# Performance work log

Hardware: AMD Instinct MI355X
Metric: run time of the kernel (lower is better)

## Reference

```python
import jax, jax.numpy as jnp
import numpy as np

D_MODEL = 1024
N_HEADS = 16
D_HEAD = 64
BATCH = 4
SEQ = 2048
NEG = -1000000000.0


def setup_inputs() -> dict:
    key = jax.random.key(0)
    k1, k2, k3, k4, k5 = jax.random.split(key, 5)
    x = jax.random.normal(k1, (BATCH, SEQ, D_MODEL), dtype=jnp.float32)
    std = 0.02
    wq = jax.random.normal(k2, (N_HEADS, D_HEAD, D_MODEL), dtype=jnp.float32) * std
    wk = jax.random.normal(k3, (N_HEADS, D_HEAD, D_MODEL), dtype=jnp.float32) * std
    wv = jax.random.normal(k4, (N_HEADS, D_HEAD, D_MODEL), dtype=jnp.float32) * std
    wo = jax.random.normal(k5, (D_MODEL, N_HEADS * D_HEAD), dtype=jnp.float32) * std
    return {"x": x, "wq": wq, "wk": wk, "wv": wv, "wo": wo}


def reference(x, wq, wk, wv, wo):
    # x: [b, s, d_model]; wq/wk/wv: [h, d_head, d_model]; wo: [d_model, h*d_head]
    b, s, _ = x.shape
    scale = jnp.sqrt(jnp.asarray(D_HEAD, x.dtype))
    q = jnp.einsum('bsd,hed->bhse', x, wq)
    k = jnp.einsum('bsd,hed->bhse', x, wk)
    v = jnp.einsum('bsd,hed->bhse', x, wv)
    scores = jnp.einsum('bhse,bhte->bhst', q, k) / scale
    causal_mask = jnp.triu(jnp.ones((s, s), dtype=bool), k=1)
    scores = jnp.where(causal_mask, jnp.asarray(NEG, scores.dtype), scores)
    weights = jax.nn.softmax(scores, axis=-1)
    heads = jnp.einsum('bhst,bhte->bhse', weights, v)  # [b, h, s, d_head]
    concat = heads.transpose(0, 2, 1, 3).reshape(b, s, N_HEADS * D_HEAD)
    return concat @ wo.T
```

## Files before the change

kernel.cpp:

```cpp
#include <hip/hip_runtime.h>


#define DEV __device__ __forceinline__

typedef __attribute__((ext_vector_type(8))) __bf16 bf16x8;
typedef __attribute__((ext_vector_type(4))) float f32x4;
typedef unsigned short u16;

struct alignas(8) U16x4 { u16 x, y, z, w; };

DEV u16 f2bf(float f) {
  unsigned int u = __builtin_bit_cast(unsigned int, f);
  u = u + 0x7FFFu + ((u >> 16) & 1u);
  return (u16)(u >> 16);
}

DEV unsigned cvt_pk_bf16(float a, float b) {
  unsigned r;
  asm("v_cvt_pk_bf16_f32 %0, %1, %2" : "=v"(r) : "v"(a), "v"(b));
  return r;
}

DEV f32x4 mfma16(uint2 a, uint2 b, f32x4 c) {
  f32x4 d;
  asm("v_mfma_f32_16x16x16_bf16 %0, %1, %2, %3" : "=v"(d) : "v"(a), "v"(b), "v"(c));
  return d;
}

DEV void gload_lds16(const void* g, void* l) {
  __builtin_amdgcn_global_load_lds(
      (const __attribute__((address_space(1))) unsigned int*)g,
      (__attribute__((address_space(3))) unsigned int*)l, 16, 0, 0);
}

DEV void waitvm(int n) {
  if (n >= 12)     asm volatile("s_waitcnt vmcnt(12)" ::: "memory");
  else if (n == 8) asm volatile("s_waitcnt vmcnt(8)" ::: "memory");
  else if (n == 4) asm volatile("s_waitcnt vmcnt(4)" ::: "memory");
  else             asm volatile("s_waitcnt vmcnt(0)" ::: "memory");
}

__global__ __launch_bounds__(256) void cast_all_kernel(
    const float* __restrict__ x, const float* __restrict__ wq,
    const float* __restrict__ wk, const float* __restrict__ wv,
    const float* __restrict__ wo, u16* __restrict__ xb,
    u16* __restrict__ wqkvb, u16* __restrict__ wob) {
  const int i = blockIdx.x * blockDim.x + threadIdx.x;
  const float* src;
  U16x4* dst;
  if (i < 2097152) {
    src = x + (size_t)i * 4;
    dst = reinterpret_cast<U16x4*>(xb) + i;
  } else if (i < 2883584) {
    const int j = i - 2097152;
    const int sel = j >> 18;
    const float* s = sel == 0 ? wq : sel == 1 ? wk : wv;
    src = s + (size_t)(j & 262143) * 4;
    dst = reinterpret_cast<U16x4*>(wqkvb) + j;
  } else {
    const int j = i - 2883584;
    src = wo + (size_t)j * 4;
    dst = reinterpret_cast<U16x4*>(wob) + j;
  }
  const float4 v = *reinterpret_cast<const float4*>(src);
  *dst = U16x4{f2bf(v.x), f2bf(v.y), f2bf(v.z), f2bf(v.w)};
}

template <int MODE, int NBN>
__global__ __launch_bounds__(256, 2) void gemm_bt(
    const u16* __restrict__ A, const u16* __restrict__ B,
    void* __restrict__ C0, u16* __restrict__ vtp, int N) {
  constexpr int K = 1024;
  const int d = blockIdx.x;
  const int chunk = gridDim.x >> 3;
  const int vg = (d & 7) * chunk + (d >> 3);
  const int bn = vg % NBN, bm = vg / NBN;
  const int tid = threadIdx.x;
  const int w = tid >> 6, lane = tid & 63, lo = lane & 15, hi = lane >> 4;
  const int wm = w >> 1, wn = w & 1;

  __shared__ char lds[65536];

  const u16* Ag = A + (size_t)(bm * 128) * K;
  const u16* Bg = B + (size_t)(bn * 128) * K;

  f32x4 acc[4][4] = {};

  auto stage = [&](int ring, int k0) {
#pragma unroll
    for (int j = 0; j < 2; ++j) {
      const int L = j * 256 + tid, r = L >> 2, c = (L & 3) ^ (r & 3);
      gload_lds16(Ag + (size_t)r * K + k0 + c * 8, lds + ring * 16384 + j * 4096 + w * 1024);
      gload_lds16(Bg + (size_t)r * K + k0 + c * 8, lds + ring * 16384 + 8192 + j * 4096 + w * 1024);
    }
  };

  stage(0, 0);
  stage(1, 32);
  stage(2, 64);

#pragma unroll
  for (int t = 0; t < 32; ++t) {
    if (t + 3 < 32) stage((t + 3) & 3, (t + 3) * 32);
    waitvm(4 * (31 - t < 3 ? 31 - t : 3));
    __builtin_amdgcn_sched_barrier(0);
    __builtin_amdgcn_s_barrier();

    const int ro = (t & 3) * 16384;
    bf16x8 af[4], bfr[4];
#pragma unroll
    for (int m = 0; m < 4; ++m) {
      const int r = wm * 64 + m * 16 + lo;
      const int p = hi ^ (lo & 3);
      af[m] = *reinterpret_cast<const bf16x8*>(lds + ro + r * 64 + p * 16);
    }
#pragma unroll
    for (int n = 0; n < 4; ++n) {
      const int r = wn * 64 + n * 16 + lo;
      const int p = hi ^ (lo & 3);
      bfr[n] = *reinterpret_cast<const bf16x8*>(lds + ro + 8192 + r * 64 + p * 16);
    }
    __builtin_amdgcn_s_setprio(1);
#pragma unroll
    for (int m = 0; m < 4; ++m)
#pragma unroll
      for (int n = 0; n < 4; ++n)
        acc[m][n] = __builtin_amdgcn_mfma_f32_16x16x32_bf16(af[m], bfr[n], acc[m][n], 0, 0, 0);
    __builtin_amdgcn_s_setprio(0);
    asm volatile("s_waitcnt lgkmcnt(0)" ::: "memory");
    __builtin_amdgcn_sched_barrier(0);
    __builtin_amdgcn_s_barrier();
  }

  const int colW = bn * 128 + wn * 64;
  const int rowW = bm * 128 + wm * 64;
  if (MODE == 0) {
    float* C = (float*)C0;
#pragma unroll
    for (int m = 0; m < 4; ++m)
#pragma unroll
      for (int n = 0; n < 4; ++n) {
        const int col = colW + n * 16 + lo;
        const int rb = rowW + m * 16 + hi * 4;
#pragma unroll
        for (int rg = 0; rg < 4; ++rg)
          C[(size_t)(rb + rg) * N + col] = acc[m][n][rg];
      }
  } else {
    u16* qkvp = (u16*)C0;
    if (bn * 128 < 2048) {
      const float qs = (bn < 8) ? 0.18033688011112042f : 1.0f;
#pragma unroll
      for (int m = 0; m < 4; ++m)
#pragma unroll
        for (int n = 0; n < 4; ++n) {
          const int col = colW + n * 16 + lo;
          const int rb = rowW + m * 16 + hi * 4;
#pragma unroll
          for (int rg = 0; rg < 4; ++rg)
            qkvp[(size_t)(rb + rg) * 2048 + col] = f2bf(acc[m][n][rg] * qs);
        }
    } else {
#pragma unroll
      for (int m = 0; m < 4; ++m)
#pragma unroll
        for (int n = 0; n < 4; ++n) {
          const int col = colW + n * 16 + lo;
          const int idx = col - 2048;
          const int hh = idx >> 6, e = idx & 63;
          const int rb = rowW + m * 16 + hi * 4;
          const int bb = rb >> 11, s = rb & 2047;
          U16x4 v4{f2bf(acc[m][n][0]), f2bf(acc[m][n][1]),
                   f2bf(acc[m][n][2]), f2bf(acc[m][n][3])};
          *reinterpret_cast<U16x4*>(vtp + ((size_t)((bb * 16 + hh) * 64 + e)) * 2048 + s) = v4;
        }
    }
  }
}

__global__ __launch_bounds__(512, 4) void attn_kernel(
    const u16* __restrict__ qkv, const u16* __restrict__ vt, u16* __restrict__ heads) {
  const int dd = blockIdx.x;
  const int vg = (dd & 7) * 64 + (dd >> 3);
  const int bx = vg & 7, bh = vg >> 3;
  const int b = bh >> 4, h = bh & 15;
  const int tid = threadIdx.x;
  const int w = tid >> 6, lane = tid & 63, lo = lane & 15, hi = lane >> 4;

  __shared__ char lds[81920];
  char* sQP = lds;
  char* sK  = lds + 16384;
  char* sV  = lds + 49152;

  const u16* Kg = qkv + (size_t)(b * 2048) * 2048 + 1024 + h * 64;
  const u16* Vg = vt + (size_t)bh * 64 * 2048;

  const int kr = tid >> 3, kc_ = (tid & 7) ^ (kr & 7);
  const int vr = tid >> 4, vc_ = (tid & 15) ^ (vr & 7);
  auto stageKV = [&](int buf, int kv0) {
#pragma unroll
    for (int it = 0; it < 2; ++it) {
      gload_lds16(Kg + (size_t)(kv0 + it * 64 + kr) * 2048 + kc_ * 8,
                  sK + buf * 16384 + it * 8192 + w * 1024);
      gload_lds16(Vg + (size_t)(it * 32 + vr) * 2048 + kv0 + vc_ * 8,
                  sV + buf * 16384 + it * 8192 + w * 1024);
    }
  };

  const int qloc = w * 16 + lo;

  for (int rep = 0; rep < 2; ++rep) {
    const int qt = rep ? (15 - bx) : bx;
    const u16* Qg = qkv + (size_t)(b * 2048 + qt * 128) * 2048 + h * 64;

#pragma unroll
    for (int it = 0; it < 2; ++it)
      gload_lds16(Qg + (size_t)(it * 64 + kr) * 2048 + kc_ * 8, sQP + it * 8192 + w * 1024);
    stageKV(0, 0);
    __syncthreads();

    bf16x8 qf[2];
#pragma unroll
    for (int kc = 0; kc < 2; ++kc) {
      const int p = (kc * 4 + hi) ^ (lo & 7);
      qf[kc] = *reinterpret_cast<const bf16x8*>(sQP + qloc * 128 + p * 16);
    }

    f32x4 lvec = {};
    f32x4 oacc[4] = {};

    const int nt = qt + 1;

    auto step = [&](int t, int cur) {
      if (t + 1 < nt) stageKV(cur ^ 1, (t + 1) * 128);
      f32x4 sa[8] = {};
      __builtin_amdgcn_s_setprio(1);
#pragma unroll
      for (int kc = 0; kc < 2; ++kc) {
#pragma unroll
        for (int n = 0; n < 8; ++n) {
          const int r = n * 16 + lo;
          const int p = (kc * 4 + hi) ^ (lo & 7);
          const bf16x8 kf = *reinterpret_cast<const bf16x8*>(sK + cur * 16384 + r * 128 + p * 16);
          sa[n] = __builtin_amdgcn_mfma_f32_16x16x32_bf16(kf, qf[kc], sa[n], 0, 0, 0);
        }
      }
      __builtin_amdgcn_s_setprio(0);

      if (t == nt - 1) {
#pragma unroll
        for (int n = 0; n < 8; ++n)
#pragma unroll
          for (int rg = 0; rg < 4; ++rg)
            if (n * 16 + hi * 4 + rg > qloc) sa[n][rg] = -1e9f;
      }

#pragma unroll
      for (int n = 0; n < 8; ++n)
#pragma unroll
        for (int rg = 0; rg < 4; ++rg) sa[n][rg] = exp2f(sa[n][rg]);
      lvec += ((sa[0] + sa[1]) + (sa[2] + sa[3])) + ((sa[4] + sa[5]) + (sa[6] + sa[7]));

      __builtin_amdgcn_s_setprio(1);
#pragma unroll
      for (int n = 0; n < 8; ++n) {
        const uint2 pb{cvt_pk_bf16(sa[n][0], sa[n][1]), cvt_pk_bf16(sa[n][2], sa[n][3])};
        const int sb = (((2 * n + (hi >> 1)) ^ (lo & 7)) << 4) + ((hi & 1) << 3);
#pragma unroll
        for (int ne = 0; ne < 4; ++ne) {
          const uint2 vf = *reinterpret_cast<const uint2*>(
              sV + cur * 16384 + (ne * 16 + lo) * 256 + sb);
          oacc[ne] = mfma16(vf, pb, oacc[ne]);
        }
      }
      __builtin_amdgcn_s_setprio(0);
      __syncthreads();
    };

    for (int i = 0; i < nt; i += 2) {
      step(i, 0);
      if (i + 1 < nt) step(i + 1, 1);
    }

    float lsum = (lvec[0] + lvec[1]) + (lvec[2] + lvec[3]);
    lsum += __shfl_xor(lsum, 16);
    lsum += __shfl_xor(lsum, 32);
    const float inv = 1.0f / lsum;
    const int q = qt * 128 + qloc;
    u16* dst = heads + (size_t)(b * 2048 + q) * 1024 + h * 64;
#pragma unroll
    for (int ne = 0; ne < 4; ++ne) {
      const unsigned r0 = cvt_pk_bf16(oacc[ne][0] * inv, oacc[ne][1] * inv);
      const unsigned r1 = cvt_pk_bf16(oacc[ne][2] * inv, oacc[ne][3] * inv);
      *reinterpret_cast<uint2*>(dst + ne * 16 + hi * 4) = uint2{r0, r1};
    }
  }
}

extern "C" void kernel_launch(void* const* d_in, const int* in_sizes, int n_in,
                              void* d_out, int out_size, void* d_ws, size_t ws_size,
                              hipStream_t stream) {
  const float* x  = (const float*)d_in[0];
  const float* wq = (const float*)d_in[1];
  const float* wk = (const float*)d_in[2];
  const float* wv = (const float*)d_in[3];
  const float* wo = (const float*)d_in[4];

  char* ws = (char*)d_ws;
  u16* xb    = (u16*)(ws);
  u16* wqkvb = (u16*)(ws + 16777216);
  u16* wob   = (u16*)(ws + 23068672);
  u16* qkv   = (u16*)(ws + 25165824);
  u16* vtp   = (u16*)(ws + 58720256);
  u16* heads = (u16*)(ws + 75497472);

  cast_all_kernel<<<12288, 256, 0, stream>>>(x, wq, wk, wv, wo, xb, wqkvb, wob);

  gemm_bt<1, 24><<<1536, 256, 0, stream>>>(xb, wqkvb, qkv, vtp, 3072);
  attn_kernel<<<512, 512, 0, stream>>>(qkv, vtp, heads);
  gemm_bt<0, 8><<<512, 256, 0, stream>>>(heads, wob, d_out, nullptr, 1024);
}
```

Before: 169.6 us.

## Rewrite attention with 32x32x16 MFMA, smaller blocks and 32-key tiles

The attention kernel is restructured to use v_mfma_f32_32x32x16_bf16 with permlane32_swap to relayout P, smaller 128-thread blocks (2048 blocks), 32-key KV tiles staged into 16KB LDS, and Q kept in registers loaded directly from global. Causal work past each wave's diagonal is skipped per wave. The goal is higher occupancy, better load balance from more, smaller blocks ordered by descending q-tile, and fewer MFMA instructions per FLOP. The cost is more barriers per unit of work, since each 32-key step now has its own sync. The GEMM waitcnt helper is also inlined.

```diff
diff --git a/kernel.cpp b/kernel.cpp
--- a/kernel.cpp
+++ b/kernel.cpp
@@ -5,6 +5,8 @@
 
 typedef __attribute__((ext_vector_type(8))) __bf16 bf16x8;
 typedef __attribute__((ext_vector_type(4))) float f32x4;
+typedef __attribute__((ext_vector_type(16))) float f32x16;
+typedef __attribute__((ext_vector_type(2))) unsigned uint32x2;
 typedef unsigned short u16;
 
 struct alignas(8) U16x4 { u16 x, y, z, w; };
@@ -21,23 +23,15 @@
   return r;
 }
 
-DEV f32x4 mfma16(uint2 a, uint2 b, f32x4 c) {
-  f32x4 d;
-  asm("v_mfma_f32_16x16x16_bf16 %0, %1, %2, %3" : "=v"(d) : "v"(a), "v"(b), "v"(c));
-  return d;
+DEV f32x16 mfma32(bf16x8 a, bf16x8 b, f32x16 c) {
+  asm("v_mfma_f32_32x32x16_bf16 %0, %1, %2, %0" : "+v"(c) : "v"(a), "v"(b));
+  return c;
 }
 
 DEV void gload_lds16(const void* g, void* l) {
   __builtin_amdgcn_global_load_lds(
       (const __attribute__((address_space(1))) unsigned int*)g,
       (__attribute__((address_space(3))) unsigned int*)l, 16, 0, 0);
-}
-
-DEV void waitvm(int n) {
-  if (n >= 12)     asm volatile("s_waitcnt vmcnt(12)" ::: "memory");
-  else if (n == 8) asm volatile("s_waitcnt vmcnt(8)" ::: "memory");
-  else if (n == 4) asm volatile("s_waitcnt vmcnt(4)" ::: "memory");
-  else             asm volatile("s_waitcnt vmcnt(0)" ::: "memory");
 }
 
 __global__ __launch_bounds__(256) void cast_all_kernel(
@@ -102,7 +96,10 @@
 #pragma unroll
   for (int t = 0; t < 32; ++t) {
     if (t + 3 < 32) stage((t + 3) & 3, (t + 3) * 32);
-    waitvm(4 * (31 - t < 3 ? 31 - t : 3));
+    if (t < 29)      asm volatile("s_waitcnt vmcnt(12)" ::: "memory");
+    else if (t == 29) asm volatile("s_waitcnt vmcnt(8)" ::: "memory");
+    else if (t == 30) asm volatile("s_waitcnt vmcnt(4)" ::: "memory");
+    else              asm volatile("s_waitcnt vmcnt(0)" ::: "memory");
     __builtin_amdgcn_sched_barrier(0);
     __builtin_amdgcn_s_barrier();
 
@@ -178,123 +175,124 @@
   }
 }
 
-__global__ __launch_bounds__(512, 4) void attn_kernel(
+__global__ __launch_bounds__(128, 4) void attn_kernel(
     const u16* __restrict__ qkv, const u16* __restrict__ vt, u16* __restrict__ heads) {
-  const int dd = blockIdx.x;
-  const int vg = (dd & 7) * 64 + (dd >> 3);
-  const int bx = vg & 7, bh = vg >> 3;
-  const int b = bh >> 4, h = bh & 15;
+  const int x = blockIdx.x & 7;
+  const int i = blockIdx.x >> 3;
+  const int bh = x + 8 * (i & 7);
+  const int qt = 31 - (i >> 3);
+  const int b = bh >> 4, hh = bh & 15;
   const int tid = threadIdx.x;
-  const int w = tid >> 6, lane = tid & 63, lo = lane & 15, hi = lane >> 4;
-
-  __shared__ char lds[81920];
-  char* sQP = lds;
-  char* sK  = lds + 16384;
-  char* sV  = lds + 49152;
-
-  const u16* Kg = qkv + (size_t)(b * 2048) * 2048 + 1024 + h * 64;
+  const int w = tid >> 6, l = tid & 63, l31 = l & 31, h = l >> 5;
+
+  __shared__ char lds[16384];
+  char* sK = lds;
+  char* sV = lds + 8192;
+
+  const u16* Kg = qkv + (size_t)(b * 2048) * 2048 + 1024 + hh * 64;
   const u16* Vg = vt + (size_t)bh * 64 * 2048;
 
-  const int kr = tid >> 3, kc_ = (tid & 7) ^ (kr & 7);
-  const int vr = tid >> 4, vc_ = (tid & 15) ^ (vr & 7);
-  auto stageKV = [&](int buf, int kv0) {
-#pragma unroll
-    for (int it = 0; it < 2; ++it) {
-      gload_lds16(Kg + (size_t)(kv0 + it * 64 + kr) * 2048 + kc_ * 8,
-                  sK + buf * 16384 + it * 8192 + w * 1024);
-      gload_lds16(Vg + (size_t)(it * 32 + vr) * 2048 + kv0 + vc_ * 8,
-                  sV + buf * 16384 + it * 8192 + w * 1024);
+  int kR[2], kC[2], vE[2], vC[2];
+#pragma unroll
+  for (int j = 0; j < 2; ++j) {
+    const int L = j * 128 + w * 64 + l;
+    kR[j] = L >> 3; kC[j] = (L & 7) ^ (kR[j] & 7);
+    vE[j] = L >> 2; vC[j] = (L & 3) ^ ((vE[j] >> 1) & 3);
+  }
+  auto stage = [&](int buf, int t) {
+    const size_t kv0 = (size_t)t * 32;
+#pragma unroll
+    for (int j = 0; j < 2; ++j) {
+      gload_lds16(Kg + (kv0 + kR[j]) * 2048 + kC[j] * 8, sK + buf * 4096 + j * 2048 + w * 1024);
+      gload_lds16(Vg + (size_t)vE[j] * 2048 + kv0 + vC[j] * 8, sV + buf * 4096 + j * 2048 + w * 1024);
     }
   };
 
-  const int qloc = w * 16 + lo;
-
-  for (int rep = 0; rep < 2; ++rep) {
-    const int qt = rep ? (15 - bx) : bx;
-    const u16* Qg = qkv + (size_t)(b * 2048 + qt * 128) * 2048 + h * 64;
-
-#pragma unroll
-    for (int it = 0; it < 2; ++it)
-      gload_lds16(Qg + (size_t)(it * 64 + kr) * 2048 + kc_ * 8, sQP + it * 8192 + w * 1024);
-    stageKV(0, 0);
-    __syncthreads();
-
-    bf16x8 qf[2];
-#pragma unroll
-    for (int kc = 0; kc < 2; ++kc) {
-      const int p = (kc * 4 + hi) ^ (lo & 7);
-      qf[kc] = *reinterpret_cast<const bf16x8*>(sQP + qloc * 128 + p * 16);
-    }
-
-    f32x4 lvec = {};
-    f32x4 oacc[4] = {};
-
-    const int nt = qt + 1;
-
-    auto step = [&](int t, int cur) {
-      if (t + 1 < nt) stageKV(cur ^ 1, (t + 1) * 128);
-      f32x4 sa[8] = {};
+  const int gq = qt * 64 + w * 32 + l31;
+  const u16* Qrow = qkv + (size_t)(b * 2048 + gq) * 2048 + hh * 64 + 8 * h;
+  bf16x8 qfr[4];
+#pragma unroll
+  for (int c = 0; c < 4; ++c)
+    qfr[c] = *reinterpret_cast<const bf16x8*>(Qrow + 16 * c);
+
+  float lsum = 0.f;
+  f32x16 oacc[2] = {};
+
+  const int nt = 2 * (qt + 1);
+  const int wqmax = qt * 64 + w * 32 + 31;
+
+  stage(0, 0);
+  __syncthreads();
+
+  auto step = [&](int t, int cur) {
+    if (t + 1 < nt) stage(cur ^ 1, t + 1);
+    if (t * 32 <= wqmax) {
+      f32x16 sa = {};
       __builtin_amdgcn_s_setprio(1);
 #pragma unroll
-      for (int kc = 0; kc < 2; ++kc) {
-#pragma unroll
-        for (int n = 0; n < 8; ++n) {
-          const int r = n * 16 + lo;
-          const int p = (kc * 4 + hi) ^ (lo & 7);
-          const bf16x8 kf = *reinterpret_cast<const bf16x8*>(sK + cur * 16384 + r * 128 + p * 16);
-          sa[n] = __builtin_amdgcn_mfma_f32_16x16x32_bf16(kf, qf[kc], sa[n], 0, 0, 0);
+      for (int c = 0; c < 4; ++c) {
+        const int slot = (2 * c + h) ^ (l31 & 7);
+        const bf16x8 kf = *reinterpret_cast<const bf16x8*>(sK + cur * 4096 + l31 * 128 + slot * 16);
+        sa = mfma32(kf, qfr[c], sa);
+      }
+      __builtin_amdgcn_s_setprio(0);
+
+      if (t >= nt - 2) {
+        const int thr = gq - t * 32;
+#pragma unroll
+        for (int r = 0; r < 16; ++r) {
+          const int rowloc = (r & 3) + 8 * (r >> 2) + 4 * h;
+          if (rowloc > thr) sa[r] = -1e9f;
         }
       }
-      __builtin_amdgcn_s_setprio(0);
-
-      if (t == nt - 1) {
-#pragma unroll
-        for (int n = 0; n < 8; ++n)
-#pragma unroll
-          for (int rg = 0; rg < 4; ++rg)
-            if (n * 16 + hi * 4 + rg > qloc) sa[n][rg] = -1e9f;
+
+#pragma unroll
+      for (int r = 0; r < 16; ++r) sa[r] = exp2f(sa[r]);
+      float rs = 0.f;
+#pragma unroll
+      for (int r = 0; r < 16; ++r) rs += sa[r];
+      lsum += rs;
+
+#pragma unroll
+      for (int sc = 0; sc < 2; ++sc) {
+        const unsigned w0 = cvt_pk_bf16(sa[8 * sc + 0], sa[8 * sc + 1]);
+        const unsigned w1 = cvt_pk_bf16(sa[8 * sc + 2], sa[8 * sc + 3]);
+        const unsigned w2 = cvt_pk_bf16(sa[8 * sc + 4], sa[8 * sc + 5]);
+        const unsigned w3 = cvt_pk_bf16(sa[8 * sc + 6], sa[8 * sc + 7]);
+        const uint32x2 s02 = __builtin_amdgcn_permlane32_swap(w0, w2, false, false);
+        const uint32x2 s13 = __builtin_amdgcn_permlane32_swap(w1, w3, false, false);
+        union { unsigned u[4]; bf16x8 v; } pb;
+        pb.u[0] = s02.x; pb.u[1] = s13.x; pb.u[2] = s02.y; pb.u[3] = s13.y;
+        __builtin_amdgcn_s_setprio(1);
+#pragma unroll
+        for (int ne = 0; ne < 2; ++ne) {
+          const int e = ne * 32 + l31;
+          const int slot = (2 * sc + h) ^ ((e >> 1) & 3);
+          const bf16x8 vf = *reinterpret_cast<const bf16x8*>(sV + cur * 4096 + e * 64 + slot * 16);
+          oacc[ne] = mfma32(vf, pb.v, oacc[ne]);
+        }
+        __builtin_amdgcn_s_setprio(0);
       }
-
-#pragma unroll
-      for (int n = 0; n < 8; ++n)
-#pragma unroll
-        for (int rg = 0; rg < 4; ++rg) sa[n][rg] = exp2f(sa[n][rg]);
-      lvec += ((sa[0] + sa[1]) + (sa[2] + sa[3])) + ((sa[4] + sa[5]) + (sa[6] + sa[7]));
-
-      __builtin_amdgcn_s_setprio(1);
-#pragma unroll
-      for (int n = 0; n < 8; ++n) {
-        const uint2 pb{cvt_pk_bf16(sa[n][0], sa[n][1]), cvt_pk_bf16(sa[n][2], sa[n][3])};
-        const int sb = (((2 * n + (hi >> 1)) ^ (lo & 7)) << 4) + ((hi & 1) << 3);
-#pragma unroll
-        for (int ne = 0; ne < 4; ++ne) {
-          const uint2 vf = *reinterpret_cast<const uint2*>(
-              sV + cur * 16384 + (ne * 16 + lo) * 256 + sb);
-          oacc[ne] = mfma16(vf, pb, oacc[ne]);
-        }
-      }
-      __builtin_amdgcn_s_setprio(0);
-      __syncthreads();
-    };
-
-    for (int i = 0; i < nt; i += 2) {
-      step(i, 0);
-      if (i + 1 < nt) step(i + 1, 1);
-    }
-
-    float lsum = (lvec[0] + lvec[1]) + (lvec[2] + lvec[3]);
-    lsum += __shfl_xor(lsum, 16);
-    lsum += __shfl_xor(lsum, 32);
-    const float inv = 1.0f / lsum;
-    const int q = qt * 128 + qloc;
-    u16* dst = heads + (size_t)(b * 2048 + q) * 1024 + h * 64;
-#pragma unroll
-    for (int ne = 0; ne < 4; ++ne) {
-      const unsigned r0 = cvt_pk_bf16(oacc[ne][0] * inv, oacc[ne][1] * inv);
-      const unsigned r1 = cvt_pk_bf16(oacc[ne][2] * inv, oacc[ne][3] * inv);
-      *reinterpret_cast<uint2*>(dst + ne * 16 + hi * 4) = uint2{r0, r1};
-    }
-  }
+    }
+    __syncthreads();
+  };
+
+  for (int t = 0; t < nt; t += 2) {
+    step(t, 0);
+    step(t + 1, 1);
+  }
+
+  const float ls = lsum + __shfl_xor(lsum, 32);
+  const float inv = 1.0f / ls;
+  u16* dst = heads + (size_t)(b * 2048 + gq) * 1024 + hh * 64;
+#pragma unroll
+  for (int ne = 0; ne < 2; ++ne)
+#pragma unroll
+    for (int r = 0; r < 16; r += 2) {
+      const int e = ne * 32 + (r & 3) + 8 * (r >> 2) + 4 * h;
+      const unsigned pkw = cvt_pk_bf16(oacc[ne][r] * inv, oacc[ne][r + 1] * inv);
+      *reinterpret_cast<unsigned*>(dst + e) = pkw;
+    }
 }
 
 extern "C" void kernel_launch(void* const* d_in, const int* in_sizes, int n_in,
@@ -317,6 +315,6 @@
   cast_all_kernel<<<12288, 256, 0, stream>>>(x, wq, wk, wv, wo, xb, wqkvb, wob);
 
   gemm_bt<1, 24><<<1536, 256, 0, stream>>>(xb, wqkvb, qkv, vtp, 3072);
-  attn_kernel<<<512, 512, 0, stream>>>(qkv, vtp, heads);
+  attn_kernel<<<2048, 128, 0, stream>>>(qkv, vtp, heads);
   gemm_bt<0, 8><<<512, 256, 0, stream>>>(heads, wob, d_out, nullptr, 1024);
 }
```

New measurement: 176.8 us. 4.2% more time.
